# Performance work log

Hardware: AMD Instinct MI355X
Metric: run time of the kernel (lower is better)

## Reference

```python
import jax, jax.numpy as jnp
import numpy as np

B, T, M = 4, 1024, 512
H, K, V = 8, 64, 64
EPS = 1e-6


def setup_inputs() -> dict:
    key = jax.random.key(0)
    ks = jax.random.split(key, 8)
    s = 1.0 / np.sqrt(M)
    return {
        "query": jax.random.normal(ks[0], (B, T, M), jnp.float32),
        "key": jax.random.normal(ks[1], (B, T, M), jnp.float32),
        "value": jax.random.normal(ks[2], (B, T, M), jnp.float32),
        "Wq": jax.random.normal(ks[3], (M, H * K), jnp.float32) * s,
        "Wk": jax.random.normal(ks[4], (M, H * K), jnp.float32) * s,
        "Wv": jax.random.normal(ks[5], (M, H * V), jnp.float32) * s,
        # gate linear is zero-initialized in the original (Constant(0.0)); use
        # small random weights so the gate path is exercised numerically.
        "Wg": jax.random.normal(ks[6], (M, H * V), jnp.float32) * (0.02 * s),
        "bg": jnp.zeros((H * V,), jnp.float32),
        "Wo": jax.random.normal(ks[7], (H * V, M), jnp.float32) * (1.0 / np.sqrt(H * V)),
    }


def _phi(x):
    return jax.nn.elu(x) + 1.0


def reference(query, key, value, Wq, Wk, Wv, Wg, bg, Wo):
    # projections -> [B, T, H, d]
    q = (query @ Wq).reshape(B, T, H, K)
    k = (key @ Wk).reshape(B, T, H, K)
    v = (value @ Wv).reshape(B, T, H, V)

    qf = _phi(q)
    kf = _phi(k)

    # multiplicative value gate from the raw value input
    gate = jax.nn.sigmoid((value @ Wg + bg).reshape(B, T, H, V))
    v = v * (2.0 * gate)

    # visualization attention map: qf . kf, causal, row-normalized
    scores = jnp.einsum("bthk,bshk->bhts", qf, kf)  # [B,H,T,T]
    causal = (jnp.arange(T)[None, :] <= jnp.arange(T)[:, None]).astype(scores.dtype)
    scores = scores * causal[None, None]
    att_map = scores / (jnp.sum(scores, axis=-1, keepdims=True) + EPS)

    # causal linear attention via cumulative sums (Tq == Tk so the idx-take
    # in the original is an identity gather)
    kv = jnp.einsum("bthk,bthv->bthkv", kf, v)  # [B,T,H,K,V]
    kv_cum = jnp.cumsum(kv, axis=1)
    k_cum = jnp.cumsum(kf, axis=1)               # [B,T,H,K]

    numer = jnp.einsum("bthk,bthkv->bthv", qf, kv_cum)
    denom = jnp.einsum("bthk,bthk->bth", qf, k_cum) + EPS
    out = (numer / denom[..., None]).reshape(B, T, H * V)
    out = out @ Wo  # [B,T,M]
    return out, att_map
```

## Files before the change

kernel.cpp:

```cpp
#include <hip/hip_runtime.h>
#include <cstdint>

#define TDIM 1024
#define BDIM 4
#define EPSF 1e-6f

#define OFF_DEN   0u
#define OFF_KSUM  32768u
#define OFF_KV    65536u
#define FLOAT_BYTES 8650752u
#define UOFF_QP 0u
#define UOFF_KP 2097152u
#define UOFF_VP 4194304u
#define UOFF_NB 6291456u
#define UOFF_WQ 8388608u
#define UOFF_WK 8650752u
#define UOFF_WV 8912896u
#define UOFF_WG 9175040u
#define UOFF_WO 9437184u

typedef short bf16x8 __attribute__((ext_vector_type(8)));
typedef float f32x4  __attribute__((ext_vector_type(4)));
typedef unsigned short ushort_t;

union bfu { int4 i4; unsigned short us[8]; bf16x8 v; };

__device__ __forceinline__ float phi_f(float x)  { return x > 0.f ? x + 1.f : __expf(x); }
__device__ __forceinline__ float sigm_f(float x) { return 1.f / (1.f + __expf(-x)); }
__device__ __forceinline__ unsigned short f2b(float x) {
    union { float f; unsigned u; } v; v.f = x;
    return (unsigned short)((v.u + 0x7FFFu + ((v.u >> 16) & 1u)) >> 16);
}
__device__ __forceinline__ float b2f(unsigned short s) {
    union { unsigned u; float f; } v; v.u = (unsigned)s << 16; return v.f;
}
__device__ __forceinline__ int4 pack8(float4 a, float4 b) {
    bfu u;
    u.us[0] = f2b(a.x); u.us[1] = f2b(a.y); u.us[2] = f2b(a.z); u.us[3] = f2b(a.w);
    u.us[4] = f2b(b.x); u.us[5] = f2b(b.y); u.us[6] = f2b(b.z); u.us[7] = f2b(b.w);
    return u.i4;
}
#define FMA4(ACC, S, V) do { (ACC).x += (S)*(V).x; (ACC).y += (S)*(V).y; \
                             (ACC).z += (S)*(V).z; (ACC).w += (S)*(V).w; } while (0)

__global__ __launch_bounds__(256) void castwt_all(const float* __restrict__ W0,
                                                  const float* __restrict__ W1,
                                                  const float* __restrict__ W2,
                                                  const float* __restrict__ W3,
                                                  const float* __restrict__ W4,
                                                  ushort_t* __restrict__ T0,
                                                  ushort_t* __restrict__ T1,
                                                  ushort_t* __restrict__ T2,
                                                  ushort_t* __restrict__ T3,
                                                  ushort_t* __restrict__ T4) {
    const float* W; ushort_t* Wt;
    switch (blockIdx.z) {
        case 0: W = W0; Wt = T0; break;
        case 1: W = W1; Wt = T1; break;
        case 2: W = W2; Wt = T2; break;
        case 3: W = W3; Wt = T3; break;
        default: W = W4; Wt = T4; break;
    }
    __shared__ unsigned short tile[32][36];
    const int t = threadIdx.x;
    const int r0 = blockIdx.y * 32, c0 = blockIdx.x * 32;
    {
        const int r = t >> 3, c4 = (t & 7) * 4;
        float4 x = *(const float4*)(W + (size_t)(r0 + r) * 512 + c0 + c4);
        tile[c4 + 0][r] = f2b(x.x); tile[c4 + 1][r] = f2b(x.y);
        tile[c4 + 2][r] = f2b(x.z); tile[c4 + 3][r] = f2b(x.w);
    }
    __syncthreads();
    const int c = t >> 3, r4 = (t & 7) * 4;
    ushort4 o;
    o.x = tile[c][r4 + 0]; o.y = tile[c][r4 + 1];
    o.z = tile[c][r4 + 2]; o.w = tile[c][r4 + 3];
    *(ushort4*)(Wt + (size_t)(c0 + c) * 512 + r0 + r4) = o;
}

template <int MODE>
__global__ __launch_bounds__(256) void mgemm_k(const void* __restrict__ Ap,
                                               const ushort_t* __restrict__ B0t,
                                               const ushort_t* __restrict__ B1t,
                                               const float* __restrict__ bias,
                                               ushort_t* __restrict__ outb,
                                               float* __restrict__ outf) {
    extern __shared__ unsigned short smem[];
    unsigned short* As  = smem;
    unsigned short* Bs  = smem + 4096;
    unsigned short* Bs2 = smem + 8192;
    const int tid  = threadIdx.x;
    const int row0 = blockIdx.x * 64;
    const int n0   = blockIdx.y * 64;
    const int w    = tid >> 6, lane = tid & 63;
    const int cc   = tid & 7,  rr   = tid >> 3;
    const int fm   = lane & 15, fq = lane >> 4;

    f32x4 acc[4], acc2[4];
#pragma unroll
    for (int i = 0; i < 4; i++) {
        acc[i]  = (f32x4){0.f, 0.f, 0.f, 0.f};
        acc2[i] = (f32x4){0.f, 0.f, 0.f, 0.f};
    }

    for (int kt = 0; kt < 512; kt += 64) {
        if (MODE == 1) {
            const ushort_t* ap = (const ushort_t*)Ap + (size_t)(row0 + rr) * 512 + kt + cc * 8;
            *(int4*)&As[(cc * 64 + (rr ^ cc)) * 8]        = *(const int4*)ap;
            *(int4*)&As[(cc * 64 + ((rr + 32) ^ cc)) * 8] = *(const int4*)(ap + 32 * 512);
        } else {
            const float* ap = (const float*)Ap + (size_t)(row0 + rr) * 512 + kt + cc * 8;
            *(int4*)&As[(cc * 64 + (rr ^ cc)) * 8] =
                pack8(*(const float4*)ap, *(const float4*)(ap + 4));
            const float* ap2 = ap + 32 * 512;
            *(int4*)&As[(cc * 64 + ((rr + 32) ^ cc)) * 8] =
                pack8(*(const float4*)ap2, *(const float4*)(ap2 + 4));
        }
        const ushort_t* bp = B0t + (size_t)(n0 + rr) * 512 + kt + cc * 8;
        *(int4*)&Bs[(cc * 64 + (rr ^ cc)) * 8]        = *(const int4*)bp;
        *(int4*)&Bs[(cc * 64 + ((rr + 32) ^ cc)) * 8] = *(const int4*)(bp + 32 * 512);
        if (MODE == 2) {
            const ushort_t* gp = B1t + (size_t)(n0 + rr) * 512 + kt + cc * 8;
            *(int4*)&Bs2[(cc * 64 + (rr ^ cc)) * 8]        = *(const int4*)gp;
            *(int4*)&Bs2[(cc * 64 + ((rr + 32) ^ cc)) * 8] = *(const int4*)(gp + 32 * 512);
        }
        __syncthreads();
#pragma unroll
        for (int j = 0; j < 2; j++) {
            const int c_ = j * 4 + fq;
            bf16x8 af = *(const bf16x8*)&As[(c_ * 64 + ((w * 16 + fm) ^ c_)) * 8];
#pragma unroll
            for (int nb = 0; nb < 4; nb++) {
                bf16x8 bfv = *(const bf16x8*)&Bs[(c_ * 64 + ((nb * 16 + fm) ^ c_)) * 8];
                acc[nb] = __builtin_amdgcn_mfma_f32_16x16x32_bf16(af, bfv, acc[nb], 0, 0, 0);
                if (MODE == 2) {
                    bf16x8 bgv = *(const bf16x8*)&Bs2[(c_ * 64 + ((nb * 16 + fm) ^ c_)) * 8];
                    acc2[nb] = __builtin_amdgcn_mfma_f32_16x16x32_bf16(af, bgv, acc2[nb], 0, 0, 0);
                }
            }
        }
        __syncthreads();
    }

#pragma unroll
    for (int nb = 0; nb < 4; nb++) {
        const int col = n0 + nb * 16 + fm;
        float bb = 0.f;
        if (MODE == 2) bb = bias[col];
#pragma unroll
        for (int r = 0; r < 4; r++) {
            const int row = row0 + w * 16 + fq * 4 + r;
            float v = acc[nb][r];
            if (MODE == 0)      outb[(size_t)row * 512 + col] = f2b(phi_f(v));
            else if (MODE == 2) outb[(size_t)row * 512 + col] =
                                    f2b(v * 2.f * sigm_f(acc2[nb][r] + bb));
            else                outf[(size_t)row * 512 + col] = v;
        }
    }
}

__global__ __launch_bounds__(256) void chunksum_k(const ushort_t* __restrict__ kb,
                                                  const ushort_t* __restrict__ vb,
                                                  float* __restrict__ kv,
                                                  float* __restrict__ ksum) {
    __shared__ __align__(16) float kf_c[64][68];
    __shared__ __align__(16) float vg_c[64][68];
    const int tid = threadIdx.x;
    const int bh = blockIdx.x, c = blockIdx.y;
    const int b = bh >> 3, h = bh & 7;
    const int r = tid >> 2, qq = tid & 3;
    {
        const size_t rowbase = ((size_t)(b * TDIM + c * 64 + r)) * 512 + h * 64 + qq * 16;
        bfu k0, k1, v0, v1;
        k0.i4 = *(const int4*)(kb + rowbase);
        k1.i4 = *(const int4*)(kb + rowbase + 8);
        v0.i4 = *(const int4*)(vb + rowbase);
        v1.i4 = *(const int4*)(vb + rowbase + 8);
#pragma unroll
        for (int j = 0; j < 8; j++) {
            kf_c[r][qq * 16 + j]     = b2f(k0.us[j]);
            kf_c[r][qq * 16 + 8 + j] = b2f(k1.us[j]);
            vg_c[r][qq * 16 + j]     = b2f(v0.us[j]);
            vg_c[r][qq * 16 + 8 + j] = b2f(v1.us[j]);
        }
    }
    __syncthreads();
    const int k0i = (tid >> 4) * 4;
    const int v0i = (tid & 15) * 4;
    float4 a4[4];
#pragma unroll
    for (int i = 0; i < 4; i++) a4[i] = make_float4(0.f, 0.f, 0.f, 0.f);
    for (int t = 0; t < 64; t++) {
        float4 kk4 = *(const float4*)&kf_c[t][k0i];
        float4 vv  = *(const float4*)&vg_c[t][v0i];
        FMA4(a4[0], kk4.x, vv); FMA4(a4[1], kk4.y, vv);
        FMA4(a4[2], kk4.z, vv); FMA4(a4[3], kk4.w, vv);
    }
    const size_t base = (size_t)(bh * 16 + c) * 64;
#pragma unroll
    for (int i = 0; i < 4; i++)
        *(float4*)(kv + (base + k0i + i) * 64 + v0i) = a4[i];
    if (tid < 64) {
        float s = 0.f;
        for (int t = 0; t < 64; t++) s += kf_c[t][tid];
        ksum[base + tid] = s;
    }
}

__global__ __launch_bounds__(256) void prefix_k(float* __restrict__ kv,
                                                float* __restrict__ ksum) {
    const int tid = threadIdx.x;
    const int bh = blockIdx.x;
    float4 run[4];
#pragma unroll
    for (int u = 0; u < 4; u++) run[u] = make_float4(0.f, 0.f, 0.f, 0.f);
    const int d0 = tid * 16;
    for (int c = 0; c < 16; c++) {
        float* p = kv + (size_t)(bh * 16 + c) * 4096 + d0;
#pragma unroll
        for (int u = 0; u < 4; u++) {
            float4 x = *(float4*)(p + 4 * u);
            *(float4*)(p + 4 * u) = run[u];
            run[u].x += x.x; run[u].y += x.y; run[u].z += x.z; run[u].w += x.w;
        }
    }
    if (tid < 64) {
        float r2 = 0.f;
        for (int c = 0; c < 16; c++) {
            float* p = ksum + (size_t)(bh * 16 + c) * 64 + tid;
            float x = *p; *p = r2; r2 += x;
        }
    }
}

__global__ __launch_bounds__(256) void chunkout_k(const ushort_t* __restrict__ qb,
                                                  const ushort_t* __restrict__ kb,
                                                  const ushort_t* __restrict__ vb,
                                                  const float* __restrict__ kvp,
                                                  const float* __restrict__ ksum,
                                                  ushort_t* __restrict__ nbo,
                                                  float* __restrict__ denom) {
    __shared__ __align__(16) unsigned short qs[4096];
    __shared__ __align__(16) unsigned short ks[4096];
    __shared__ __align__(16) unsigned short vs[4096];
    __shared__ __align__(16) unsigned short kvs[4096];
    __shared__ __align__(16) float sc[64][68];
    __shared__ __align__(16) float kpre[64];
    __shared__ __align__(16) float ps[64][4];
    __shared__ __align__(16) float inv_s[64];
    const int tid = threadIdx.x;
    const int bh = blockIdx.x, c = blockIdx.y;
    const int b = bh >> 3, h = bh & 7;
    const int w = tid >> 6, lane = tid & 63;
    const int fm = lane & 15, fq = lane >> 4;

    {
        const int rr = tid >> 3, cc = tid & 7;
        const ushort_t* qp = qb + ((size_t)(b * TDIM + c * 64 + rr)) * 512 + h * 64 + cc * 8;
        const ushort_t* kp = kb + ((size_t)(b * TDIM + c * 64 + rr)) * 512 + h * 64 + cc * 8;
        *(int4*)&qs[(cc * 64 + (rr ^ cc)) * 8]        = *(const int4*)qp;
        *(int4*)&qs[(cc * 64 + ((rr + 32) ^ cc)) * 8] = *(const int4*)(qp + 32 * 512);
        *(int4*)&ks[(cc * 64 + (rr ^ cc)) * 8]        = *(const int4*)kp;
        *(int4*)&ks[(cc * 64 + ((rr + 32) ^ cc)) * 8] = *(const int4*)(kp + 32 * 512);
        const int v = tid & 63, su0 = (tid >> 6) * 2;
#pragma unroll
        for (int e = 0; e < 2; e++) {
            const int su = su0 + e;
            bfu t1;
#pragma unroll
            for (int j = 0; j < 8; j++)
                t1.us[j] = vb[((size_t)(b * TDIM + c * 64 + su * 8 + j)) * 512 + h * 64 + v];
            *(int4*)&vs[(su * 64 + (v ^ su)) * 8] = t1.i4;
            bfu t2;
            const float* kvrow = kvp + (size_t)(bh * 16 + c) * 4096 + v;
#pragma unroll
            for (int j = 0; j < 8; j++)
                t2.us[j] = f2b(kvrow[(su * 8 + j) * 64]);
            *(int4*)&kvs[(su * 64 + (v ^ su)) * 8] = t2.i4;
        }
        if (tid < 64) kpre[tid] = ksum[(size_t)(bh * 16 + c) * 64 + tid];
    }
    __syncthreads();

    {
        f32x4 sa[4];
#pragma unroll
        for (int i = 0; i < 4; i++) sa[i] = (f32x4){0.f, 0.f, 0.f, 0.f};
#pragma unroll
        for (int j = 0; j < 2; j++) {
            const int cu = j * 4 + fq;
            bf16x8 aq = *(const bf16x8*)&qs[(cu * 64 + ((w * 16 + fm) ^ cu)) * 8];
#pragma unroll
            for (int nb = 0; nb < 4; nb++) {
                bf16x8 bk = *(const bf16x8*)&ks[(cu * 64 + ((nb * 16 + fm) ^ cu)) * 8];
                sa[nb] = __builtin_amdgcn_mfma_f32_16x16x32_bf16(aq, bk, sa[nb], 0, 0, 0);
            }
        }
#pragma unroll
        for (int nb = 0; nb < 4; nb++) {
            const int s_l = nb * 16 + fm;
#pragma unroll
            for (int r = 0; r < 4; r++) {
                const int t_l = w * 16 + fq * 4 + r;
                sc[t_l][s_l] = (s_l <= t_l) ? sa[nb][r] : 0.f;
            }
        }
    }
    __syncthreads();

    {
        const int rw = tid >> 2, sq = tid & 3;
        float p = 0.f;
#pragma unroll
        for (int s = sq * 16; s < sq * 16 + 16; s++) p += sc[rw][s];
#pragma unroll
        for (int kd = sq * 16; kd < sq * 16 + 16; kd++) {
            const int cu = kd >> 3;
            p += b2f(qs[(cu * 64 + (rw ^ cu)) * 8 + (kd & 7)]) * kpre[kd];
        }
        ps[rw][sq] = p;
    }
    __syncthreads();
    {
        const int rw = tid >> 2, sq = tid & 3;
        if (sq == 0) {
            float den = ps[rw][0] + ps[rw][1] + ps[rw][2] + ps[rw][3];
            denom[(size_t)bh * TDIM + c * 64 + rw] = den;
            inv_s[rw] = 1.f / (den + EPSF);
        }
    }
    __syncthreads();

    {
        f32x4 oa[4];
#pragma unroll
        for (int i = 0; i < 4; i++) oa[i] = (f32x4){0.f, 0.f, 0.f, 0.f};
        bf16x8 aq[2], ap_[2];
#pragma unroll
        for (int j = 0; j < 2; j++) {
            const int cu = j * 4 + fq;
            aq[j] = *(const bf16x8*)&qs[(cu * 64 + ((w * 16 + fm) ^ cu)) * 8];
            bfu t;
#pragma unroll
            for (int e2 = 0; e2 < 8; e2++) t.us[e2] = f2b(sc[w * 16 + fm][cu * 8 + e2]);
            ap_[j] = t.v;
        }
#pragma unroll
        for (int nb = 0; nb < 4; nb++) {
#pragma unroll
            for (int j = 0; j < 2; j++) {
                const int cu = j * 4 + fq;
                bf16x8 bkv = *(const bf16x8*)&kvs[(cu * 64 + ((nb * 16 + fm) ^ cu)) * 8];
                bf16x8 bv  = *(const bf16x8*)&vs[(cu * 64 + ((nb * 16 + fm) ^ cu)) * 8];
                oa[nb] = __builtin_amdgcn_mfma_f32_16x16x32_bf16(aq[j], bkv, oa[nb], 0, 0, 0);
                oa[nb] = __builtin_amdgcn_mfma_f32_16x16x32_bf16(ap_[j], bv, oa[nb], 0, 0, 0);
            }
        }
#pragma unroll
        for (int nb = 0; nb < 4; nb++) {
            const int vcol = nb * 16 + fm;
#pragma unroll
            for (int r = 0; r < 4; r++) {
                const int t_l = w * 16 + fq * 4 + r;
                const float val = oa[nb][r] * inv_s[t_l];
                nbo[((size_t)(b * TDIM + c * 64 + t_l)) * 512 + h * 64 + vcol] = f2b(val);
            }
        }
    }
}

__global__ __launch_bounds__(256) void attmap_k(const ushort_t* __restrict__ qb,
                                                const ushort_t* __restrict__ kb,
                                                const float* __restrict__ denom,
                                                float* __restrict__ att) {
    __shared__ __align__(16) unsigned short qs[4096];
    __shared__ __align__(16) unsigned short ks[4096];
    __shared__ __align__(16) float inv_s[64];
    const int tid = threadIdx.x;
    const int bh = blockIdx.x, diag = blockIdx.y;
    const int tt0 = diag * 64;
    const int b = bh >> 3, h = bh & 7;
    const int w = tid >> 6, lane = tid & 63;
    const int fm = lane & 15, fq = lane >> 4;
    const int rr = tid >> 3, cc = tid & 7;
    {
        const ushort_t* qp = qb + ((size_t)(b * TDIM + tt0 + rr)) * 512 + h * 64 + cc * 8;
        *(int4*)&qs[(cc * 64 + (rr ^ cc)) * 8]        = *(const int4*)qp;
        *(int4*)&qs[(cc * 64 + ((rr + 32) ^ cc)) * 8] = *(const int4*)(qp + 32 * 512);
        if (tid < 64) inv_s[tid] = 1.f / (denom[(size_t)bh * TDIM + tt0 + tid] + EPSF);
    }
    float* attb = att + (size_t)bh * TDIM * TDIM;
    for (int st = 0; st <= diag; st++) {
        const int s0 = st * 64;
        const ushort_t* kp = kb + ((size_t)(b * TDIM + s0 + rr)) * 512 + h * 64 + cc * 8;
        __syncthreads();
        *(int4*)&ks[(cc * 64 + (rr ^ cc)) * 8]        = *(const int4*)kp;
        *(int4*)&ks[(cc * 64 + ((rr + 32) ^ cc)) * 8] = *(const int4*)(kp + 32 * 512);
        __syncthreads();
        f32x4 sa[4];
#pragma unroll
        for (int i = 0; i < 4; i++) sa[i] = (f32x4){0.f, 0.f, 0.f, 0.f};
#pragma unroll
        for (int j = 0; j < 2; j++) {
            const int cu = j * 4 + fq;
            bf16x8 aq = *(const bf16x8*)&qs[(cu * 64 + ((w * 16 + fm) ^ cu)) * 8];
#pragma unroll
            for (int nb = 0; nb < 4; nb++) {
                bf16x8 bk = *(const bf16x8*)&ks[(cu * 64 + ((nb * 16 + fm) ^ cu)) * 8];
                sa[nb] = __builtin_amdgcn_mfma_f32_16x16x32_bf16(aq, bk, sa[nb], 0, 0, 0);
            }
        }
#pragma unroll
        for (int nb = 0; nb < 4; nb++) {
            const int s_g = s0 + nb * 16 + fm;
#pragma unroll
            for (int r = 0; r < 4; r++) {
                const int t_l = w * 16 + fq * 4 + r;
                const int t_g = tt0 + t_l;
                const float val = (s_g <= t_g) ? sa[nb][r] * inv_s[t_l] : 0.f;
                attb[(size_t)t_g * TDIM + s_g] = val;
            }
        }
    }
    {
        const float4 z = make_float4(0.f, 0.f, 0.f, 0.f);
        const int r = tid >> 2, qq = tid & 3;
        float* rowp = attb + (size_t)(tt0 + r) * TDIM;
        for (int c0 = (diag + 1) * 64 + qq * 4; c0 < TDIM; c0 += 16)
            *(float4*)(rowp + c0) = z;
    }
}

extern "C" void kernel_launch(void* const* d_in, const int* in_sizes, int n_in,
                              void* d_out, int out_size, void* d_ws, size_t ws_size,
                              hipStream_t stream) {
    (void)in_sizes; (void)n_in; (void)out_size; (void)ws_size;
    const float* query = (const float*)d_in[0];
    const float* key   = (const float*)d_in[1];
    const float* value = (const float*)d_in[2];
    const float* Wq    = (const float*)d_in[3];
    const float* Wk    = (const float*)d_in[4];
    const float* Wv    = (const float*)d_in[5];
    const float* Wg    = (const float*)d_in[6];
    const float* bg    = (const float*)d_in[7];
    const float* Wo    = (const float*)d_in[8];
    float* out = (float*)d_out;
    float* att = (float*)d_out + 2097152;
    float* ws  = (float*)d_ws;
    float* den  = ws + OFF_DEN;
    float* ksum = ws + OFF_KSUM;
    float* kv   = ws + OFF_KV;
    ushort_t* ub  = (ushort_t*)((char*)d_ws + FLOAT_BYTES);
    ushort_t* qp  = ub + UOFF_QP;
    ushort_t* kp  = ub + UOFF_KP;
    ushort_t* vp  = ub + UOFF_VP;
    ushort_t* nbp = ub + UOFF_NB;
    ushort_t* wqt = ub + UOFF_WQ;
    ushort_t* wkt = ub + UOFF_WK;
    ushort_t* wvt = ub + UOFF_WV;
    ushort_t* wgt = ub + UOFF_WG;
    ushort_t* wot = ub + UOFF_WO;

    dim3 blk(256);
    castwt_all<<<dim3(16, 16, 5), blk, 0, stream>>>(Wq, Wk, Wv, Wg, Wo,
                                                    wqt, wkt, wvt, wgt, wot);
    dim3 ggrid(64, 8);
    mgemm_k<0><<<ggrid, blk, 16384, stream>>>(query, wqt, nullptr, nullptr, qp, nullptr);
    mgemm_k<0><<<ggrid, blk, 16384, stream>>>(key,   wkt, nullptr, nullptr, kp, nullptr);
    mgemm_k<2><<<ggrid, blk, 24576, stream>>>(value, wvt, wgt, bg, vp, nullptr);
    chunksum_k<<<dim3(32, 16), blk, 0, stream>>>(kp, vp, kv, ksum);
    prefix_k<<<dim3(32), blk, 0, stream>>>(kv, ksum);
    chunkout_k<<<dim3(32, 16), blk, 0, stream>>>(qp, kp, vp, kv, ksum, nbp, den);
    attmap_k<<<dim3(32, 16), blk, 0, stream>>>(qp, kp, den, att);
    mgemm_k<1><<<ggrid, blk, 16384, stream>>>(nbp, wot, nullptr, nullptr, nullptr, out);
}
```

Before: 284.3 us.

## Double-buffer GEMM and attmap K tiles, merge QKV projections, use nontemporal stores

Merges the three input projection GEMMs into one launch indexed by blockIdx.z, and double-buffers the shared-memory A/B tiles with register prefetch so global loads overlap MFMA work. The output projection and the attention-map kernel get the same prefetch/double-buffer scheme, which removes one barrier per K step. The attention-map kernel also hoists the Q fragments and inverse denominators into registers, skips the causal mask on off-diagonal tiles, and writes the large att output with nontemporal stores. In exchange, shared memory per block doubles, which may lower occupancy, and the runtime dual branch in the merged projection kernel adds some divergence-free overhead.

Result: faster. 266.1 us (-6.4%).

```diff
diff --git a/kernel.cpp b/kernel.cpp
--- a/kernel.cpp
+++ b/kernel.cpp
@@ -78,23 +78,33 @@
     *(ushort4*)(Wt + (size_t)(c0 + c) * 512 + r0 + r4) = o;
 }
 
-template <int MODE>
-__global__ __launch_bounds__(256) void mgemm_k(const void* __restrict__ Ap,
-                                               const ushort_t* __restrict__ B0t,
-                                               const ushort_t* __restrict__ B1t,
-                                               const float* __restrict__ bias,
-                                               ushort_t* __restrict__ outb,
-                                               float* __restrict__ outf) {
-    extern __shared__ unsigned short smem[];
-    unsigned short* As  = smem;
-    unsigned short* Bs  = smem + 4096;
-    unsigned short* Bs2 = smem + 8192;
-    const int tid  = threadIdx.x;
-    const int row0 = blockIdx.x * 64;
-    const int n0   = blockIdx.y * 64;
-    const int w    = tid >> 6, lane = tid & 63;
-    const int cc   = tid & 7,  rr   = tid >> 3;
-    const int fm   = lane & 15, fq = lane >> 4;
+__global__ __launch_bounds__(256) void proj_k(const float* __restrict__ query,
+                                              const float* __restrict__ key_,
+                                              const float* __restrict__ value,
+                                              const ushort_t* __restrict__ wqt,
+                                              const ushort_t* __restrict__ wkt,
+                                              const ushort_t* __restrict__ wvt,
+                                              const ushort_t* __restrict__ wgt,
+                                              const float* __restrict__ bg,
+                                              ushort_t* __restrict__ qp,
+                                              ushort_t* __restrict__ kp,
+                                              ushort_t* __restrict__ vp) {
+    __shared__ __align__(16) unsigned short As[2][4096];
+    __shared__ __align__(16) unsigned short Bs[2][4096];
+    __shared__ __align__(16) unsigned short Bs2[2][4096];
+    const int z = blockIdx.z;
+    const float* A = (z == 0) ? query : (z == 1) ? key_ : value;
+    const ushort_t* B0 = (z == 0) ? wqt : (z == 1) ? wkt : wvt;
+    ushort_t* outp = (z == 0) ? qp : (z == 1) ? kp : vp;
+    const bool dual = (z == 2);
+
+    const int tid = threadIdx.x;
+    const int row0 = blockIdx.x * 64, n0 = blockIdx.y * 64;
+    const int w = tid >> 6, lane = tid & 63;
+    const int cc = tid & 7, rr = tid >> 3;
+    const int fm = lane & 15, fq = lane >> 4;
+    const int la0 = (cc * 64 + (rr ^ cc)) * 8;
+    const int la1 = (cc * 64 + ((rr + 32) ^ cc)) * 8;
 
     f32x4 acc[4], acc2[4];
 #pragma unroll
@@ -103,58 +113,149 @@
         acc2[i] = (f32x4){0.f, 0.f, 0.f, 0.f};
     }
 
-    for (int kt = 0; kt < 512; kt += 64) {
-        if (MODE == 1) {
-            const ushort_t* ap = (const ushort_t*)Ap + (size_t)(row0 + rr) * 512 + kt + cc * 8;
-            *(int4*)&As[(cc * 64 + (rr ^ cc)) * 8]        = *(const int4*)ap;
-            *(int4*)&As[(cc * 64 + ((rr + 32) ^ cc)) * 8] = *(const int4*)(ap + 32 * 512);
+    const float*   aptr = A  + (size_t)(row0 + rr) * 512 + cc * 8;
+    const ushort_t* bptr = B0 + (size_t)(n0 + rr) * 512 + cc * 8;
+    const ushort_t* gptr = wgt + (size_t)(n0 + rr) * 512 + cc * 8;
+
+    float4 a0 = *(const float4*)(aptr);
+    float4 a1 = *(const float4*)(aptr + 4);
+    float4 a2 = *(const float4*)(aptr + 32 * 512);
+    float4 a3 = *(const float4*)(aptr + 32 * 512 + 4);
+    int4 b0 = *(const int4*)(bptr);
+    int4 b1 = *(const int4*)(bptr + 32 * 512);
+    int4 g0 = {0, 0, 0, 0}, g1 = {0, 0, 0, 0};
+    if (dual) { g0 = *(const int4*)(gptr); g1 = *(const int4*)(gptr + 32 * 512); }
+    *(int4*)&As[0][la0] = pack8(a0, a1);
+    *(int4*)&As[0][la1] = pack8(a2, a3);
+    *(int4*)&Bs[0][la0] = b0; *(int4*)&Bs[0][la1] = b1;
+    if (dual) { *(int4*)&Bs2[0][la0] = g0; *(int4*)&Bs2[0][la1] = g1; }
+    __syncthreads();
+
+    for (int kti = 0; kti < 8; kti++) {
+        const int buf = kti & 1;
+        if (kti < 7) {
+            const int off = (kti + 1) * 64;
+            a0 = *(const float4*)(aptr + off);
+            a1 = *(const float4*)(aptr + off + 4);
+            a2 = *(const float4*)(aptr + off + 32 * 512);
+            a3 = *(const float4*)(aptr + off + 32 * 512 + 4);
+            b0 = *(const int4*)(bptr + off);
+            b1 = *(const int4*)(bptr + off + 32 * 512);
+            if (dual) {
+                g0 = *(const int4*)(gptr + off);
+                g1 = *(const int4*)(gptr + off + 32 * 512);
+            }
+        }
+        if (dual) {
+#pragma unroll
+            for (int j = 0; j < 2; j++) {
+                const int cu = j * 4 + fq;
+                bf16x8 af = *(const bf16x8*)&As[buf][(cu * 64 + ((w * 16 + fm) ^ cu)) * 8];
+#pragma unroll
+                for (int nb = 0; nb < 4; nb++) {
+                    bf16x8 bv = *(const bf16x8*)&Bs[buf][(cu * 64 + ((nb * 16 + fm) ^ cu)) * 8];
+                    bf16x8 gv = *(const bf16x8*)&Bs2[buf][(cu * 64 + ((nb * 16 + fm) ^ cu)) * 8];
+                    acc[nb]  = __builtin_amdgcn_mfma_f32_16x16x32_bf16(af, bv, acc[nb], 0, 0, 0);
+                    acc2[nb] = __builtin_amdgcn_mfma_f32_16x16x32_bf16(af, gv, acc2[nb], 0, 0, 0);
+                }
+            }
         } else {
-            const float* ap = (const float*)Ap + (size_t)(row0 + rr) * 512 + kt + cc * 8;
-            *(int4*)&As[(cc * 64 + (rr ^ cc)) * 8] =
-                pack8(*(const float4*)ap, *(const float4*)(ap + 4));
-            const float* ap2 = ap + 32 * 512;
-            *(int4*)&As[(cc * 64 + ((rr + 32) ^ cc)) * 8] =
-                pack8(*(const float4*)ap2, *(const float4*)(ap2 + 4));
-        }
-        const ushort_t* bp = B0t + (size_t)(n0 + rr) * 512 + kt + cc * 8;
-        *(int4*)&Bs[(cc * 64 + (rr ^ cc)) * 8]        = *(const int4*)bp;
-        *(int4*)&Bs[(cc * 64 + ((rr + 32) ^ cc)) * 8] = *(const int4*)(bp + 32 * 512);
-        if (MODE == 2) {
-            const ushort_t* gp = B1t + (size_t)(n0 + rr) * 512 + kt + cc * 8;
-            *(int4*)&Bs2[(cc * 64 + (rr ^ cc)) * 8]        = *(const int4*)gp;
-            *(int4*)&Bs2[(cc * 64 + ((rr + 32) ^ cc)) * 8] = *(const int4*)(gp + 32 * 512);
-        }
-        __syncthreads();
-#pragma unroll
-        for (int j = 0; j < 2; j++) {
-            const int c_ = j * 4 + fq;
-            bf16x8 af = *(const bf16x8*)&As[(c_ * 64 + ((w * 16 + fm) ^ c_)) * 8];
-#pragma unroll
-            for (int nb = 0; nb < 4; nb++) {
-                bf16x8 bfv = *(const bf16x8*)&Bs[(c_ * 64 + ((nb * 16 + fm) ^ c_)) * 8];
-                acc[nb] = __builtin_amdgcn_mfma_f32_16x16x32_bf16(af, bfv, acc[nb], 0, 0, 0);
-                if (MODE == 2) {
-                    bf16x8 bgv = *(const bf16x8*)&Bs2[(c_ * 64 + ((nb * 16 + fm) ^ c_)) * 8];
-                    acc2[nb] = __builtin_amdgcn_mfma_f32_16x16x32_bf16(af, bgv, acc2[nb], 0, 0, 0);
+#pragma unroll
+            for (int j = 0; j < 2; j++) {
+                const int cu = j * 4 + fq;
+                bf16x8 af = *(const bf16x8*)&As[buf][(cu * 64 + ((w * 16 + fm) ^ cu)) * 8];
+#pragma unroll
+                for (int nb = 0; nb < 4; nb++) {
+                    bf16x8 bv = *(const bf16x8*)&Bs[buf][(cu * 64 + ((nb * 16 + fm) ^ cu)) * 8];
+                    acc[nb] = __builtin_amdgcn_mfma_f32_16x16x32_bf16(af, bv, acc[nb], 0, 0, 0);
                 }
             }
         }
-        __syncthreads();
+        if (kti < 7) {
+            const int nb_ = buf ^ 1;
+            *(int4*)&As[nb_][la0] = pack8(a0, a1);
+            *(int4*)&As[nb_][la1] = pack8(a2, a3);
+            *(int4*)&Bs[nb_][la0] = b0; *(int4*)&Bs[nb_][la1] = b1;
+            if (dual) { *(int4*)&Bs2[nb_][la0] = g0; *(int4*)&Bs2[nb_][la1] = g1; }
+            __syncthreads();
+        }
     }
 
 #pragma unroll
     for (int nb = 0; nb < 4; nb++) {
         const int col = n0 + nb * 16 + fm;
-        float bb = 0.f;
-        if (MODE == 2) bb = bias[col];
+        const float bb = dual ? bg[col] : 0.f;
 #pragma unroll
         for (int r = 0; r < 4; r++) {
             const int row = row0 + w * 16 + fq * 4 + r;
-            float v = acc[nb][r];
-            if (MODE == 0)      outb[(size_t)row * 512 + col] = f2b(phi_f(v));
-            else if (MODE == 2) outb[(size_t)row * 512 + col] =
-                                    f2b(v * 2.f * sigm_f(acc2[nb][r] + bb));
-            else                outf[(size_t)row * 512 + col] = v;
+            const float v = acc[nb][r];
+            const ushort_t o = dual ? f2b(v * 2.f * sigm_f(acc2[nb][r] + bb))
+                                    : f2b(phi_f(v));
+            outp[(size_t)row * 512 + col] = o;
+        }
+    }
+}
+
+__global__ __launch_bounds__(256) void outproj_k(const ushort_t* __restrict__ A,
+                                                 const ushort_t* __restrict__ Bt,
+                                                 float* __restrict__ out) {
+    __shared__ __align__(16) unsigned short As[2][4096];
+    __shared__ __align__(16) unsigned short Bs[2][4096];
+    const int tid = threadIdx.x;
+    const int row0 = blockIdx.x * 64, n0 = blockIdx.y * 64;
+    const int w = tid >> 6, lane = tid & 63;
+    const int cc = tid & 7, rr = tid >> 3;
+    const int fm = lane & 15, fq = lane >> 4;
+    const int la0 = (cc * 64 + (rr ^ cc)) * 8;
+    const int la1 = (cc * 64 + ((rr + 32) ^ cc)) * 8;
+
+    f32x4 acc[4];
+#pragma unroll
+    for (int i = 0; i < 4; i++) acc[i] = (f32x4){0.f, 0.f, 0.f, 0.f};
+
+    const ushort_t* aptr = A  + (size_t)(row0 + rr) * 512 + cc * 8;
+    const ushort_t* bptr = Bt + (size_t)(n0 + rr) * 512 + cc * 8;
+    int4 ra0 = *(const int4*)(aptr);
+    int4 ra1 = *(const int4*)(aptr + 32 * 512);
+    int4 rb0 = *(const int4*)(bptr);
+    int4 rb1 = *(const int4*)(bptr + 32 * 512);
+    *(int4*)&As[0][la0] = ra0; *(int4*)&As[0][la1] = ra1;
+    *(int4*)&Bs[0][la0] = rb0; *(int4*)&Bs[0][la1] = rb1;
+    __syncthreads();
+
+    for (int kti = 0; kti < 8; kti++) {
+        const int buf = kti & 1;
+        if (kti < 7) {
+            const int off = (kti + 1) * 64;
+            ra0 = *(const int4*)(aptr + off);
+            ra1 = *(const int4*)(aptr + off + 32 * 512);
+            rb0 = *(const int4*)(bptr + off);
+            rb1 = *(const int4*)(bptr + off + 32 * 512);
+        }
+#pragma unroll
+        for (int j = 0; j < 2; j++) {
+            const int cu = j * 4 + fq;
+            bf16x8 af = *(const bf16x8*)&As[buf][(cu * 64 + ((w * 16 + fm) ^ cu)) * 8];
+#pragma unroll
+            for (int nb = 0; nb < 4; nb++) {
+                bf16x8 bv = *(const bf16x8*)&Bs[buf][(cu * 64 + ((nb * 16 + fm) ^ cu)) * 8];
+                acc[nb] = __builtin_amdgcn_mfma_f32_16x16x32_bf16(af, bv, acc[nb], 0, 0, 0);
+            }
+        }
+        if (kti < 7) {
+            const int nb_ = buf ^ 1;
+            *(int4*)&As[nb_][la0] = ra0; *(int4*)&As[nb_][la1] = ra1;
+            *(int4*)&Bs[nb_][la0] = rb0; *(int4*)&Bs[nb_][la1] = rb1;
+            __syncthreads();
+        }
+    }
+#pragma unroll
+    for (int nb = 0; nb < 4; nb++) {
+        const int col = n0 + nb * 16 + fm;
+#pragma unroll
+        for (int r = 0; r < 4; r++) {
+            const int row = row0 + w * 16 + fq * 4 + r;
+            __builtin_nontemporal_store(acc[nb][r], &out[(size_t)row * 512 + col]);
         }
     }
 }
@@ -374,7 +475,7 @@
                                                 const float* __restrict__ denom,
                                                 float* __restrict__ att) {
     __shared__ __align__(16) unsigned short qs[4096];
-    __shared__ __align__(16) unsigned short ks[4096];
+    __shared__ __align__(16) unsigned short ks[2][4096];
     __shared__ __align__(16) float inv_s[64];
     const int tid = threadIdx.x;
     const int bh = blockIdx.x, diag = blockIdx.y;
@@ -383,51 +484,85 @@
     const int w = tid >> 6, lane = tid & 63;
     const int fm = lane & 15, fq = lane >> 4;
     const int rr = tid >> 3, cc = tid & 7;
-    {
-        const ushort_t* qp = qb + ((size_t)(b * TDIM + tt0 + rr)) * 512 + h * 64 + cc * 8;
-        *(int4*)&qs[(cc * 64 + (rr ^ cc)) * 8]        = *(const int4*)qp;
-        *(int4*)&qs[(cc * 64 + ((rr + 32) ^ cc)) * 8] = *(const int4*)(qp + 32 * 512);
-        if (tid < 64) inv_s[tid] = 1.f / (denom[(size_t)bh * TDIM + tt0 + tid] + EPSF);
-    }
+    const int la0 = (cc * 64 + (rr ^ cc)) * 8;
+    const int la1 = (cc * 64 + ((rr + 32) ^ cc)) * 8;
+
+    const ushort_t* qptr = qb + ((size_t)(b * TDIM + tt0 + rr)) * 512 + h * 64 + cc * 8;
+    const ushort_t* kbase = kb + ((size_t)(b * TDIM + rr)) * 512 + h * 64 + cc * 8;
+    *(int4*)&qs[la0] = *(const int4*)qptr;
+    *(int4*)&qs[la1] = *(const int4*)(qptr + 32 * 512);
+    int4 rk0 = *(const int4*)(kbase);
+    int4 rk1 = *(const int4*)(kbase + 32 * 512);
+    *(int4*)&ks[0][la0] = rk0;
+    *(int4*)&ks[0][la1] = rk1;
+    if (tid < 64) inv_s[tid] = 1.f / (denom[(size_t)bh * TDIM + tt0 + tid] + EPSF);
+    __syncthreads();
+
+    bf16x8 aq[2];
+    float invr[4];
+#pragma unroll
+    for (int j = 0; j < 2; j++) {
+        const int cu = j * 4 + fq;
+        aq[j] = *(const bf16x8*)&qs[(cu * 64 + ((w * 16 + fm) ^ cu)) * 8];
+    }
+#pragma unroll
+    for (int r = 0; r < 4; r++) invr[r] = inv_s[w * 16 + fq * 4 + r];
+
     float* attb = att + (size_t)bh * TDIM * TDIM;
     for (int st = 0; st <= diag; st++) {
-        const int s0 = st * 64;
-        const ushort_t* kp = kb + ((size_t)(b * TDIM + s0 + rr)) * 512 + h * 64 + cc * 8;
-        __syncthreads();
-        *(int4*)&ks[(cc * 64 + (rr ^ cc)) * 8]        = *(const int4*)kp;
-        *(int4*)&ks[(cc * 64 + ((rr + 32) ^ cc)) * 8] = *(const int4*)(kp + 32 * 512);
-        __syncthreads();
+        const int buf = st & 1;
+        if (st < diag) {
+            const size_t off = (size_t)(st + 1) * 64 * 512;
+            rk0 = *(const int4*)(kbase + off);
+            rk1 = *(const int4*)(kbase + off + 32 * 512);
+        }
         f32x4 sa[4];
 #pragma unroll
         for (int i = 0; i < 4; i++) sa[i] = (f32x4){0.f, 0.f, 0.f, 0.f};
 #pragma unroll
         for (int j = 0; j < 2; j++) {
             const int cu = j * 4 + fq;
-            bf16x8 aq = *(const bf16x8*)&qs[(cu * 64 + ((w * 16 + fm) ^ cu)) * 8];
 #pragma unroll
             for (int nb = 0; nb < 4; nb++) {
-                bf16x8 bk = *(const bf16x8*)&ks[(cu * 64 + ((nb * 16 + fm) ^ cu)) * 8];
-                sa[nb] = __builtin_amdgcn_mfma_f32_16x16x32_bf16(aq, bk, sa[nb], 0, 0, 0);
-            }
-        }
-#pragma unroll
-        for (int nb = 0; nb < 4; nb++) {
-            const int s_g = s0 + nb * 16 + fm;
-#pragma unroll
-            for (int r = 0; r < 4; r++) {
-                const int t_l = w * 16 + fq * 4 + r;
-                const int t_g = tt0 + t_l;
-                const float val = (s_g <= t_g) ? sa[nb][r] * inv_s[t_l] : 0.f;
-                attb[(size_t)t_g * TDIM + s_g] = val;
-            }
-        }
-    }
-    {
-        const float4 z = make_float4(0.f, 0.f, 0.f, 0.f);
+                bf16x8 bk = *(const bf16x8*)&ks[buf][(cu * 64 + ((nb * 16 + fm) ^ cu)) * 8];
+                sa[nb] = __builtin_amdgcn_mfma_f32_16x16x32_bf16(aq[j], bk, sa[nb], 0, 0, 0);
+            }
+        }
+        const int s0 = st * 64;
+        if (st < diag) {
+#pragma unroll
+            for (int nb = 0; nb < 4; nb++) {
+                const int s_g = s0 + nb * 16 + fm;
+#pragma unroll
+                for (int r = 0; r < 4; r++) {
+                    const int t_g = tt0 + w * 16 + fq * 4 + r;
+                    __builtin_nontemporal_store(sa[nb][r] * invr[r],
+                                                &attb[(size_t)t_g * TDIM + s_g]);
+                }
+            }
+            *(int4*)&ks[buf ^ 1][la0] = rk0;
+            *(int4*)&ks[buf ^ 1][la1] = rk1;
+            __syncthreads();
+        } else {
+#pragma unroll
+            for (int nb = 0; nb < 4; nb++) {
+                const int s_l = nb * 16 + fm;
+#pragma unroll
+                for (int r = 0; r < 4; r++) {
+                    const int t_l = w * 16 + fq * 4 + r;
+                    const float val = (s_l <= t_l) ? sa[nb][r] * invr[r] : 0.f;
+                    __builtin_nontemporal_store(val,
+                        &attb[(size_t)(tt0 + t_l) * TDIM + s0 + s_l]);
+                }
+            }
+        }
+    }
+    {
+        const f32x4 z = (f32x4){0.f, 0.f, 0.f, 0.f};
         const int r = tid >> 2, qq = tid & 3;
         float* rowp = attb + (size_t)(tt0 + r) * TDIM;
         for (int c0 = (diag + 1) * 64 + qq * 4; c0 < TDIM; c0 += 16)
-            *(float4*)(rowp + c0) = z;
+            __builtin_nontemporal_store(z, (f32x4*)(rowp + c0));
     }
 }
 
@@ -464,13 +599,11 @@
     dim3 blk(256);
     castwt_all<<<dim3(16, 16, 5), blk, 0, stream>>>(Wq, Wk, Wv, Wg, Wo,
                                                     wqt, wkt, wvt, wgt, wot);
-    dim3 ggrid(64, 8);
-    mgemm_k<0><<<ggrid, blk, 16384, stream>>>(query, wqt, nullptr, nullptr, qp, nullptr);
-    mgemm_k<0><<<ggrid, blk, 16384, stream>>>(key,   wkt, nullptr, nullptr, kp, nullptr);
-    mgemm_k<2><<<ggrid, blk, 24576, stream>>>(value, wvt, wgt, bg, vp, nullptr);
+    proj_k<<<dim3(64, 8, 3), blk, 0, stream>>>(query, key, value,
+                                               wqt, wkt, wvt, wgt, bg, qp, kp, vp);
     chunksum_k<<<dim3(32, 16), blk, 0, stream>>>(kp, vp, kv, ksum);
     prefix_k<<<dim3(32), blk, 0, stream>>>(kv, ksum);
     chunkout_k<<<dim3(32, 16), blk, 0, stream>>>(qp, kp, vp, kv, ksum, nbp, den);
     attmap_k<<<dim3(32, 16), blk, 0, stream>>>(qp, kp, den, att);
-    mgemm_k<1><<<ggrid, blk, 16384, stream>>>(nbp, wot, nullptr, nullptr, nullptr, out);
-}
+    outproj_k<<<dim3(64, 8), blk, 0, stream>>>(nbp, wot, out);
+}
```
